# Kernel tuning notes

Measured on AMD Instinct MI355X. Metric: run time of the kernel, lower is better.

The kernel has to match this reference:

```python
import jax, jax.numpy as jnp
import numpy as np
import math

D_MODEL = 1024
N_HEADS = 16
D_HEAD = D_MODEL // N_HEADS
B, L = 4, 2048


def setup_inputs() -> dict:
    key = jax.random.key(0)
    ks = jax.random.split(key, 9)
    s = 1.0 / math.sqrt(D_MODEL)
    x = jax.random.normal(ks[0], (B, L, D_MODEL), dtype=jnp.float32)
    # causal mask, broadcastable over batch and heads
    attn_mask = jnp.tril(jnp.ones((L, L), dtype=jnp.int32))[None, None, :, :]
    Wq = jax.random.uniform(ks[1], (D_MODEL, D_MODEL), jnp.float32, -s, s)
    bq = jax.random.uniform(ks[2], (D_MODEL,), jnp.float32, -s, s)
    Wk = jax.random.uniform(ks[3], (D_MODEL, D_MODEL), jnp.float32, -s, s)
    bk = jax.random.uniform(ks[4], (D_MODEL,), jnp.float32, -s, s)
    Wv = jax.random.uniform(ks[5], (D_MODEL, D_MODEL), jnp.float32, -s, s)
    bv = jax.random.uniform(ks[6], (D_MODEL,), jnp.float32, -s, s)
    Wo = jax.random.uniform(ks[7], (D_MODEL, D_MODEL), jnp.float32, -s, s)
    bo = jax.random.uniform(ks[8], (D_MODEL,), jnp.float32, -s, s)
    return {"x": x, "attn_mask": attn_mask, "Wq": Wq, "bq": bq, "Wk": Wk,
            "bk": bk, "Wv": Wv, "bv": bv, "Wo": Wo, "bo": bo}


def reference(x, attn_mask, Wq, bq, Wk, bk, Wv, bv, Wo, bo):
    Bn, Ln, Dn = x.shape
    scale = 1.0 / math.sqrt(D_HEAD)

    def split_heads(t):  # [B,L,D] -> [B,H,L,dh]
        return t.reshape(Bn, Ln, N_HEADS, D_HEAD).transpose(0, 2, 1, 3)

    q = split_heads(x @ Wq + bq)
    k = split_heads(x @ Wk + bk)
    v = split_heads(x @ Wv + bv)
    scores = jnp.einsum('bhqd,bhkd->bhqk', q, k) * scale
    scores = jnp.where(attn_mask == 0, jnp.float32(-jnp.inf), scores)
    attn = jax.nn.softmax(scores, axis=-1)  # dropout p=0.0 -> identity
    ctx = jnp.einsum('bhqk,bhkd->bhqd', attn, v)
    ctx = ctx.transpose(0, 2, 1, 3).reshape(Bn, Ln, Dn)
    return ctx @ Wo + bo
```

## Files before the change

kernel.cpp:

```cpp
#include <hip/hip_runtime.h>


typedef unsigned short u16;
typedef __attribute__((ext_vector_type(8))) short short8;
typedef __attribute__((ext_vector_type(4))) float floatx4;
typedef __attribute__((ext_vector_type(2))) unsigned int uint2v;

#define NEG_BIG (-1e30f)
#define SCL_LOG2E 0.1803368801111244f

__device__ __forceinline__ u16 f2bf(float f) {
  unsigned int u = __builtin_bit_cast(unsigned int, f);
  u += 0x7fffu + ((u >> 16) & 1u);
  return (u16)(u >> 16);
}

__device__ __forceinline__ float max3f(float a, float b, float c) {
  float d;
  asm("v_max3_f32 %0, %1, %2, %3" : "=v"(d) : "v"(a), "v"(b), "v"(c));
  return d;
}

__device__ __forceinline__ short8 cvt8(const float* __restrict__ p) {
  const floatx4 a = *(const floatx4*)p;
  const floatx4 b = *(const floatx4*)(p + 4);
  short8 r;
  r[0] = (short)f2bf(a[0]); r[1] = (short)f2bf(a[1]);
  r[2] = (short)f2bf(a[2]); r[3] = (short)f2bf(a[3]);
  r[4] = (short)f2bf(b[0]); r[5] = (short)f2bf(b[1]);
  r[6] = (short)f2bf(b[2]); r[7] = (short)f2bf(b[3]);
  return r;
}

__device__ __forceinline__ void gll16(const u16* g, u16* l) {
  __builtin_amdgcn_global_load_lds((const __attribute__((address_space(1))) void*)g,
                                   (__attribute__((address_space(3))) void*)l,
                                   16, 0, 0);
}

__global__ void prep(const float* __restrict__ x, u16* __restrict__ xb,
                     const float* __restrict__ s0, const float* __restrict__ s1,
                     const float* __restrict__ s2, const float* __restrict__ s3,
                     u16* __restrict__ d0, u16* __restrict__ d1,
                     u16* __restrict__ d2, u16* __restrict__ d3) {
  const int t = threadIdx.x;
  if (blockIdx.z >= 4) {
    const int rid = (blockIdx.z - 4) * 256 + blockIdx.y * 16 + blockIdx.x;
#pragma unroll
    for (int i = 0; i < 8; ++i) {
      const size_t idx = (size_t)rid * 16384 + i * 2048 + t * 8;
      *(short8*)(xb + idx) = cvt8(x + idx);
    }
    return;
  }
  __shared__ u16 tile[64][72];
  const float* src; u16* dst;
  switch (blockIdx.z) {
    case 0: src = s0; dst = d0; break;
    case 1: src = s1; dst = d1; break;
    case 2: src = s2; dst = d2; break;
    default: src = s3; dst = d3; break;
  }
  const int c = t & 63, rg = t >> 6;
  const int x0 = blockIdx.x * 64, y0 = blockIdx.y * 64;
#pragma unroll
  for (int i = 0; i < 16; ++i) {
    const int row = rg * 16 + i;
    tile[row][c] = f2bf(src[(size_t)(y0 + row) * 1024 + x0 + c]);
  }
  __syncthreads();
#pragma unroll
  for (int i = 0; i < 16; ++i) {
    const int row = rg * 16 + i;
    dst[(size_t)(x0 + row) * 1024 + y0 + c] = tile[c][row];
  }
}

__global__ void transpose_v(const u16* __restrict__ Vb, u16* __restrict__ Vt) {
  __shared__ u16 tile[64][66];
  const int bh = blockIdx.y;
  const int l0 = blockIdx.x * 64;
  const size_t base = (size_t)bh * (2048 * 64);
  const int t = threadIdx.x;
#pragma unroll
  for (int c = t; c < 512; c += 256) {
    const int row = c >> 3, cc = c & 7;
    *(short8*)&tile[row][cc * 8] =
        *(const short8*)(Vb + base + (size_t)(l0 + row) * 64 + cc * 8);
  }
  __syncthreads();
  const int c2 = t & 63, rg = t >> 6;
#pragma unroll
  for (int i = 0; i < 16; ++i) {
    const int dr = rg * 16 + i;
    Vt[base + (size_t)dr * 2048 + l0 + c2] = tile[c2][dr];
  }
}

__global__ __launch_bounds__(256, 2) void gemm_qkv(
    const u16* __restrict__ A, const u16* __restrict__ Bt,
    const float* __restrict__ bq, const float* __restrict__ bk,
    const float* __restrict__ bv,
    u16* __restrict__ Qb, u16* __restrict__ Kb, u16* __restrict__ Vb) {
  const int K = 1024;
  __shared__ __align__(16) u16 As[128 * 32];
  __shared__ __align__(16) u16 Bs[128 * 32];
  const int t = threadIdx.x;
  const int w = t >> 6, l = t & 63;
  const int quad = l >> 4, l16 = l & 15;
  const int lin = blockIdx.y * 24 + blockIdx.x;
  const int nl = (lin & 7) * 192 + (lin >> 3);
  const int m0 = (nl / 24) * 128, n0 = (nl % 24) * 128;
  const int wr = w >> 1, wc = w & 1;

  floatx4 acc[4][4] = {};

  for (int k0 = 0; k0 < K; k0 += 32) {
    __syncthreads();
#pragma unroll
    for (int p = 0; p < 2; ++p) {
      const int c0 = (p * 4 + w) * 64;
      const int c = c0 + l;
      const int row = c >> 2;
      const int koff = (c & 3) * 8;
      gll16(A + (size_t)(m0 + row) * K + k0 + koff, &As[c0 * 8]);
      gll16(Bt + (size_t)(n0 + row) * K + k0 + koff, &Bs[c0 * 8]);
    }
    __syncthreads();

    short8 af[4], bf[4];
#pragma unroll
    for (int i = 0; i < 4; ++i)
      af[i] = *(const short8*)&As[(wr * 64 + i * 16 + l16) * 32 + quad * 8];
#pragma unroll
    for (int j = 0; j < 4; ++j)
      bf[j] = *(const short8*)&Bs[(wc * 64 + j * 16 + l16) * 32 + quad * 8];
#pragma unroll
    for (int i = 0; i < 4; ++i)
#pragma unroll
      for (int j = 0; j < 4; ++j)
        acc[i][j] = __builtin_amdgcn_mfma_f32_16x16x32_bf16(af[i], bf[j], acc[i][j], 0, 0, 0);
  }

  const int seg = n0 >> 10;
  const float* bias = (seg == 0) ? bq : (seg == 1) ? bk : bv;
  u16* dst = (seg == 0) ? Qb : (seg == 1) ? Kb : Vb;
  const float scl = (seg == 0) ? SCL_LOG2E : 1.0f;
#pragma unroll
  for (int j = 0; j < 4; ++j) {
    const int nn = (n0 & 1023) + wc * 64 + j * 16 + l16;
    const float bvs = bias[nn];
    const int h = nn >> 6, dh = nn & 63;
#pragma unroll
    for (int i = 0; i < 4; ++i) {
      const int rb = m0 + wr * 64 + i * 16 + quad * 4;
#pragma unroll
      for (int r = 0; r < 4; ++r) {
        const int m = rb + r;
        const int b = m >> 11, ll = m & 2047;
        dst[((size_t)(b * 16 + h) * 2048 + ll) * 64 + dh] = f2bf((acc[i][j][r] + bvs) * scl);
      }
    }
  }
}

__global__ __launch_bounds__(256, 2) void gemm_out(
    const u16* __restrict__ A, const u16* __restrict__ Bt,
    const float* __restrict__ bias, float* __restrict__ C, int M, int N, int K) {
  __shared__ __align__(16) u16 As[128 * 32];
  __shared__ __align__(16) u16 Bs[128 * 32];
  const int t = threadIdx.x;
  const int w = t >> 6, l = t & 63;
  const int quad = l >> 4, l16 = l & 15;
  const int lin = blockIdx.y * 8 + blockIdx.x;
  const int nl = (lin & 7) * 64 + (lin >> 3);
  const int m0 = (nl >> 3) * 128, n0 = (nl & 7) * 128;
  const int wr = w >> 1, wc = w & 1;

  floatx4 acc[4][4] = {};

  for (int k0 = 0; k0 < K; k0 += 32) {
    __syncthreads();
#pragma unroll
    for (int p = 0; p < 2; ++p) {
      const int c0 = (p * 4 + w) * 64;
      const int c = c0 + l;
      const int row = c >> 2;
      const int koff = (c & 3) * 8;
      gll16(A + (size_t)(m0 + row) * K + k0 + koff, &As[c0 * 8]);
      gll16(Bt + (size_t)(n0 + row) * K + k0 + koff, &Bs[c0 * 8]);
    }
    __syncthreads();

    short8 af[4], bf[4];
#pragma unroll
    for (int i = 0; i < 4; ++i)
      af[i] = *(const short8*)&As[(wr * 64 + i * 16 + l16) * 32 + quad * 8];
#pragma unroll
    for (int j = 0; j < 4; ++j)
      bf[j] = *(const short8*)&Bs[(wc * 64 + j * 16 + l16) * 32 + quad * 8];
#pragma unroll
    for (int i = 0; i < 4; ++i)
#pragma unroll
      for (int j = 0; j < 4; ++j)
        acc[i][j] = __builtin_amdgcn_mfma_f32_16x16x32_bf16(af[i], bf[j], acc[i][j], 0, 0, 0);
  }

#pragma unroll
  for (int j = 0; j < 4; ++j) {
    const int n = n0 + wc * 64 + j * 16 + l16;
    const float bvs = bias[n];
#pragma unroll
    for (int i = 0; i < 4; ++i) {
      const int rb = m0 + wr * 64 + i * 16 + quad * 4;
#pragma unroll
      for (int r = 0; r < 4; ++r)
        C[(size_t)(rb + r) * N + n] = acc[i][j][r] + bvs;
    }
  }
}

__global__ __launch_bounds__(512, 4) void attn_kernel(
    const u16* __restrict__ Q, const u16* __restrict__ K,
    const u16* __restrict__ Vt, u16* __restrict__ ctx) {
  __shared__ __align__(16) u16 Ks[2][64 * 64];
  __shared__ __align__(16) u16 Vs[2][64 * 64];
  __shared__ __align__(16) u16 Ps[8 * 16 * 64];

  const int t = threadIdx.x;
  const int w = t >> 6, l = t & 63;
  const int quad = l >> 4, l16 = l & 15;
  const int lin = blockIdx.y * 8 + blockIdx.x;
  const int bh = (lin & 7) * 8 + ((lin >> 3) & 7);
  const int pp = lin >> 6;
  const size_t base = (size_t)bh * (2048 * 64);
  const int b = bh >> 4, h = bh & 15;
  u16* Pw = &Ps[w * 16 * 64];
  unsigned int* Pw32 = (unsigned int*)Pw;

  const short8 vone = {(short)0x3F80, (short)0x3F80, (short)0x3F80, (short)0x3F80,
                       (short)0x3F80, (short)0x3F80, (short)0x3F80, (short)0x3F80};

  const int pc = w * 64 + l;
  const int sr = pc >> 3, sc = (pc & 7) ^ (sr & 7);
  const int swz = (l16 & 7);

  auto run_seg = [&](int p) {
    const int q0 = p * 128;
    const int nkt = 2 * p + 2;
    const int qg = q0 + w * 16 + l16;
    const int qmax = q0 + w * 16 + 15;
    const int qmin = q0 + w * 16;

    short8 aq[2];
#pragma unroll
    for (int ks = 0; ks < 2; ++ks)
      aq[ks] = *(const short8*)(Q + base + (size_t)qg * 64 + ks * 32 + quad * 8);

    gll16(K + base + (size_t)sr * 64 + sc * 8, &Ks[0][(w * 64) * 8]);
    gll16(Vt + base + (size_t)sr * 2048 + sc * 8, &Vs[0][(w * 64) * 8]);

    floatx4 o[4] = {};
    floatx4 lacc = {};
    float mrun = 0.f;
    floatx4 mneg = {};

    for (int kt = 0; kt < nkt; ++kt) {
      const int cur = kt & 1, nxt = cur ^ 1;
      __syncthreads();
      if (kt + 1 < nkt) {
        const int kn = (kt + 1) * 64;
        gll16(K + base + (size_t)(kn + sr) * 64 + sc * 8, &Ks[nxt][(w * 64) * 8]);
        gll16(Vt + base + (size_t)sr * 2048 + kn + sc * 8, &Vs[nxt][(w * 64) * 8]);
      }
      const int kbase = kt * 64;
      if (kbase > qmax) continue;
      const bool masked = (kbase + 63 > qmin);

      floatx4 s[4];
      __builtin_amdgcn_s_setprio(1);
#pragma unroll
      for (int tn = 0; tn < 4; ++tn) {
        const short8 bk = *(const short8*)&Ks[cur][(tn * 16 + l16) * 64 + ((quad ^ swz) << 3)];
        s[tn] = __builtin_amdgcn_mfma_f32_16x16x32_bf16(bk, aq[0], mneg, 0, 0, 0);
      }
#pragma unroll
      for (int tn = 0; tn < 4; ++tn) {
        const short8 bk = *(const short8*)&Ks[cur][(tn * 16 + l16) * 64 + (((4 + quad) ^ swz) << 3)];
        s[tn] = __builtin_amdgcn_mfma_f32_16x16x32_bf16(bk, aq[1], s[tn], 0, 0, 0);
      }
      __builtin_amdgcn_s_setprio(0);

      if (masked) {
#pragma unroll
        for (int tn = 0; tn < 4; ++tn)
#pragma unroll
          for (int r = 0; r < 4; ++r)
            if (kbase + tn * 16 + quad * 4 + r > qg) s[tn][r] = NEG_BIG;
      }
      const float m0t = max3f(s[0][0], s[0][1], s[0][2]);
      const float m1t = max3f(s[0][3], s[1][0], s[1][1]);
      const float m2t = max3f(s[1][2], s[1][3], s[2][0]);
      const float m3t = max3f(s[2][1], s[2][2], s[2][3]);
      const float m4t = max3f(s[3][0], s[3][1], s[3][2]);
      float mx = fmaxf(max3f(m0t, m1t, m2t), max3f(m3t, m4t, s[3][3]));
      mx = fmaxf(mx, __shfl_xor(mx, 16));
      mx = fmaxf(mx, __shfl_xor(mx, 32));

      if (!__all(mx <= 8.f)) {
        const float mxp = fmaxf(mx, 0.f);
        const float al = exp2f(-mxp);
        mrun += mxp;
        mneg[0] = -mrun; mneg[1] = -mrun; mneg[2] = -mrun; mneg[3] = -mrun;
#pragma unroll
        for (int tn = 0; tn < 4; ++tn)
#pragma unroll
          for (int r = 0; r < 4; ++r) s[tn][r] -= mxp;
#pragma unroll
        for (int r = 0; r < 4; ++r) lacc[r] *= al;
#pragma unroll
        for (int td = 0; td < 4; ++td)
#pragma unroll
          for (int r = 0; r < 4; ++r) o[td][r] *= al;
      }

#pragma unroll
      for (int tn = 0; tn < 4; ++tn)
#pragma unroll
        for (int r = 0; r < 4; ++r)
          s[tn][r] = exp2f(s[tn][r]);

#pragma unroll
      for (int tn = 0; tn < 4; ++tn) {
        unsigned int p0, p1;
        asm("v_cvt_pk_bf16_f32 %0, %1, %2"
            : "=v"(p0) : "v"(s[tn][0]), "v"(s[tn][1]));
        asm("v_cvt_pk_bf16_f32 %0, %1, %2"
            : "=v"(p1) : "v"(s[tn][2]), "v"(s[tn][3]));
        const int cc = (2 * tn + (quad >> 1)) ^ swz;
        uint2v pr; pr.x = p0; pr.y = p1;
        *(uint2v*)&Pw32[l16 * 32 + cc * 4 + 2 * (quad & 1)] = pr;
      }
      __asm__ volatile("s_waitcnt lgkmcnt(0)" ::: "memory");
      __builtin_amdgcn_wave_barrier();

      short8 ap[2];
#pragma unroll
      for (int ks = 0; ks < 2; ++ks)
        ap[ks] = *(const short8*)&Pw[l16 * 64 + (((ks * 4 + quad) ^ swz) << 3)];

      __builtin_amdgcn_s_setprio(1);
      lacc = __builtin_amdgcn_mfma_f32_16x16x32_bf16(vone, ap[0], lacc, 0, 0, 0);
      lacc = __builtin_amdgcn_mfma_f32_16x16x32_bf16(vone, ap[1], lacc, 0, 0, 0);
#pragma unroll
      for (int ks = 0; ks < 2; ++ks)
#pragma unroll
        for (int td = 0; td < 4; ++td) {
          const short8 bv = *(const short8*)&Vs[cur][(td * 16 + l16) * 64 + (((ks * 4 + quad) ^ swz) << 3)];
          o[td] = __builtin_amdgcn_mfma_f32_16x16x32_bf16(bv, ap[ks], o[td], 0, 0, 0);
        }
      __builtin_amdgcn_s_setprio(0);
    }

    const float inv = 1.f / lacc[0];
    u16* crow = ctx + ((size_t)(b * 2048 + qg)) * 1024 + h * 64;
#pragma unroll
    for (int td = 0; td < 4; ++td) {
      unsigned int lo, hi;
      asm("v_cvt_pk_bf16_f32 %0, %1, %2"
          : "=v"(lo) : "v"(o[td][0] * inv), "v"(o[td][1] * inv));
      asm("v_cvt_pk_bf16_f32 %0, %1, %2"
          : "=v"(hi) : "v"(o[td][2] * inv), "v"(o[td][3] * inv));
      uint2v pk;
      pk.x = lo; pk.y = hi;
      *(uint2v*)(crow + td * 16 + quad * 4) = pk;
    }
  };

  run_seg(15 - pp);
  __syncthreads();
  run_seg(pp);
}

extern "C" void kernel_launch(void* const* d_in, const int* in_sizes, int n_in,
                              void* d_out, int out_size, void* d_ws, size_t ws_size,
                              hipStream_t stream) {
  const float* x  = (const float*)d_in[0];
  const float* Wq = (const float*)d_in[2];
  const float* bq = (const float*)d_in[3];
  const float* Wk = (const float*)d_in[4];
  const float* bk = (const float*)d_in[5];
  const float* Wv = (const float*)d_in[6];
  const float* bv = (const float*)d_in[7];
  const float* Wo = (const float*)d_in[8];
  const float* bo = (const float*)d_in[9];

  u16* ws = (u16*)d_ws;
  const size_t WSZ = 1u << 20;
  const size_t TSZ = 8u << 20;
  u16* WqT = ws;
  u16* WkT = ws + WSZ;
  u16* WvT = ws + 2 * WSZ;
  u16* WoT = ws + 3 * WSZ;
  u16* xb  = ws + 4 * WSZ;
  u16* Qb  = xb + TSZ;
  u16* Kb  = Qb + TSZ;
  u16* Vb  = Kb + TSZ;
  u16* Vtb = xb;
  u16* Ctx = Vb;

  const dim3 tb(256);
  prep<<<dim3(16, 16, 6), tb, 0, stream>>>(x, xb, Wq, Wk, Wv, Wo, WqT, WkT, WvT, WoT);
  gemm_qkv<<<dim3(24, 64), tb, 0, stream>>>(xb, WqT, bq, bk, bv, Qb, Kb, Vb);
  transpose_v<<<dim3(32, 64), tb, 0, stream>>>(Vb, Vtb);
  attn_kernel<<<dim3(8, 64), dim3(512), 0, stream>>>(Qb, Kb, Vtb, Ctx);
  gemm_out<<<dim3(8, 64), tb, 0, stream>>>(Ctx, WoT, bo, (float*)d_out, 8192, 1024, 1024);
}
```

Baseline: 291.9 us.

## Deepen K/V prefetch to distance two with four-slot LDS ring

New measurement: 279.9 us. 4.1% less time.

```diff
diff --git a/kernel.cpp b/kernel.cpp
--- a/kernel.cpp
+++ b/kernel.cpp
@@ -223,8 +223,8 @@
 __global__ __launch_bounds__(512, 4) void attn_kernel(
     const u16* __restrict__ Q, const u16* __restrict__ K,
     const u16* __restrict__ Vt, u16* __restrict__ ctx) {
-  __shared__ __align__(16) u16 Ks[2][64 * 64];
-  __shared__ __align__(16) u16 Vs[2][64 * 64];
+  __shared__ __align__(16) u16 KsA[4 * 4096];
+  __shared__ __align__(16) u16 VsA[4 * 4096];
   __shared__ __align__(16) u16 Ps[8 * 16 * 64];
 
   const int t = threadIdx.x;
@@ -244,21 +244,25 @@
   const int pc = w * 64 + l;
   const int sr = pc >> 3, sc = (pc & 7) ^ (sr & 7);
   const int swz = (l16 & 7);
+  const int wk = w * 512;
+  const u16* kg0 = K + base + (size_t)sr * 64 + sc * 8;
+  const u16* vg0 = Vt + base + (size_t)sr * 2048 + sc * 8;
 
   auto run_seg = [&](int p) {
     const int q0 = p * 128;
     const int nkt = 2 * p + 2;
     const int qg = q0 + w * 16 + l16;
     const int qmax = q0 + w * 16 + 15;
-    const int qmin = q0 + w * 16;
 
     short8 aq[2];
 #pragma unroll
     for (int ks = 0; ks < 2; ++ks)
       aq[ks] = *(const short8*)(Q + base + (size_t)qg * 64 + ks * 32 + quad * 8);
 
-    gll16(K + base + (size_t)sr * 64 + sc * 8, &Ks[0][(w * 64) * 8]);
-    gll16(Vt + base + (size_t)sr * 2048 + sc * 8, &Vs[0][(w * 64) * 8]);
+    gll16(kg0, &KsA[0 * 4096 + wk]);
+    gll16(vg0, &VsA[0 * 4096 + wk]);
+    gll16(kg0 + 4096, &KsA[1 * 4096 + wk]);
+    gll16(vg0 + 64, &VsA[1 * 4096 + wk]);
 
     floatx4 o[4] = {};
     floatx4 lacc = {};
@@ -266,27 +270,33 @@
     floatx4 mneg = {};
 
     for (int kt = 0; kt < nkt; ++kt) {
-      const int cur = kt & 1, nxt = cur ^ 1;
-      __syncthreads();
-      if (kt + 1 < nkt) {
-        const int kn = (kt + 1) * 64;
-        gll16(K + base + (size_t)(kn + sr) * 64 + sc * 8, &Ks[nxt][(w * 64) * 8]);
-        gll16(Vt + base + (size_t)sr * 2048 + kn + sc * 8, &Vs[nxt][(w * 64) * 8]);
-      }
+      const int cb = (kt & 3) * 4096;
+      if (kt + 2 < nkt) {
+        const int nb = ((kt + 2) & 3) * 4096;
+        gll16(kg0 + (size_t)(kt + 2) * 4096, &KsA[nb + wk]);
+        gll16(vg0 + (kt + 2) * 64, &VsA[nb + wk]);
+        asm volatile("s_waitcnt vmcnt(4)" ::: "memory");
+      } else if (kt + 1 < nkt) {
+        asm volatile("s_waitcnt vmcnt(2)" ::: "memory");
+      } else {
+        asm volatile("s_waitcnt vmcnt(0)" ::: "memory");
+      }
+      __builtin_amdgcn_s_barrier();
+
       const int kbase = kt * 64;
       if (kbase > qmax) continue;
-      const bool masked = (kbase + 63 > qmin);
+      const bool masked = (kbase + 63 > q0 + w * 16);
 
       floatx4 s[4];
       __builtin_amdgcn_s_setprio(1);
 #pragma unroll
       for (int tn = 0; tn < 4; ++tn) {
-        const short8 bk = *(const short8*)&Ks[cur][(tn * 16 + l16) * 64 + ((quad ^ swz) << 3)];
+        const short8 bk = *(const short8*)&KsA[cb + (tn * 16 + l16) * 64 + ((quad ^ swz) << 3)];
         s[tn] = __builtin_amdgcn_mfma_f32_16x16x32_bf16(bk, aq[0], mneg, 0, 0, 0);
       }
 #pragma unroll
       for (int tn = 0; tn < 4; ++tn) {
-        const short8 bk = *(const short8*)&Ks[cur][(tn * 16 + l16) * 64 + (((4 + quad) ^ swz) << 3)];
+        const short8 bk = *(const short8*)&KsA[cb + (tn * 16 + l16) * 64 + (((4 + quad) ^ swz) << 3)];
         s[tn] = __builtin_amdgcn_mfma_f32_16x16x32_bf16(bk, aq[1], s[tn], 0, 0, 0);
       }
       __builtin_amdgcn_s_setprio(0);
@@ -356,7 +366,7 @@
       for (int ks = 0; ks < 2; ++ks)
 #pragma unroll
         for (int td = 0; td < 4; ++td) {
-          const short8 bv = *(const short8*)&Vs[cur][(td * 16 + l16) * 64 + (((ks * 4 + quad) ^ swz) << 3)];
+          const short8 bv = *(const short8*)&VsA[cb + (td * 16 + l16) * 64 + (((ks * 4 + quad) ^ swz) << 3)];
           o[td] = __builtin_amdgcn_mfma_f32_16x16x32_bf16(bv, ap[ks], o[td], 0, 0, 0);
         }
       __builtin_amdgcn_s_setprio(0);
```
